# Optimization experiments

Measured on AMD Instinct MI355X. Metric: run time of the kernel, lower is better.

Reference implementation:

```python
import jax, jax.numpy as jnp
import numpy as np

B, F, L = 256, 32, 4096  # batch, num_filters, length == input_dim


def setup_inputs() -> dict:
    key = jax.random.key(0)
    k1, k2, k3 = jax.random.split(key, 3)
    x = jax.random.normal(k1, (B, L), dtype=jnp.float32)
    window_params = jax.random.normal(k2, (F, L), dtype=jnp.float32) * 0.02
    # original init: linspace(0.1, 0.5, F).unsqueeze(0); use same deterministic init
    freq_params = jnp.linspace(0.1, 0.5, F, dtype=jnp.float32)[None, :]
    return {"x": x, "window_params": window_params, "freq_params": freq_params}


def reference(x, window_params, freq_params):
    # x: [B, L]; window_params: [F, L]; freq_params: [1, F]
    length = x.shape[-1]
    windows = jax.nn.softmax(window_params, axis=-1)            # [F, L]
    freqs = jax.nn.sigmoid(freq_params)[0] * 0.5                # [F]
    n = jnp.arange(length, dtype=jnp.float32)                   # [L]
    # complex modulation atoms for ALL filters at once (single batched FFT)
    phase = -2.0 * jnp.pi * freqs[:, None] * n[None, :]         # [F, L]
    modulation = jnp.exp(1j * phase.astype(jnp.complex64))      # [F, L] complex64
    atoms = windows.astype(jnp.complex64) * modulation          # [F, L]
    Xf = jnp.fft.fft(x, axis=-1)                                # [B, L]
    Af = jnp.fft.fft(atoms, axis=-1)                            # [F, L]
    # circular correlation of x with each atom, all filters batched
    prod = Xf[:, None, :] * jnp.conj(Af)[None, :, :]            # [B, F, L]
    return jnp.real(jnp.fft.ifft(prod, axis=-1)).astype(x.dtype)  # [B, F, L]
```

## Files before the change

### kernel.cpp

```cpp
#include <hip/hip_runtime.h>
#include <math.h>

#define B 256
#define F 32
#define L 4096
#define NT 256
#define TWO_PI 6.28318530717958647692f

__device__ __forceinline__ int pidx(int i) { return i + (i >> 4); }

__device__ __forceinline__ int rev3(int i) {
    return ((i & 15) << 8) | (i & 0xF0) | (i >> 8);
}

__device__ __forceinline__ float2 cmul(float2 a, float2 b) {
    return make_float2(a.x * b.x - a.y * b.y, a.x * b.y + a.y * b.x);
}
__device__ __forceinline__ float2 cmulc(float2 a, float cr, float ci) {
    return make_float2(a.x * cr - a.y * ci, a.x * ci + a.y * cr);
}

template<int SGN>
__device__ __forceinline__ void dft4(float2& a, float2& b, float2& c, float2& d) {
    const float s = (float)SGN;
    float2 t0 = make_float2(a.x + c.x, a.y + c.y);
    float2 t1 = make_float2(a.x - c.x, a.y - c.y);
    float2 t2 = make_float2(b.x + d.x, b.y + d.y);
    float2 t3 = make_float2(b.x - d.x, b.y - d.y);
    float2 it3 = make_float2(-s * t3.y, s * t3.x);
    a = make_float2(t0.x + t2.x, t0.y + t2.y);
    c = make_float2(t0.x - t2.x, t0.y - t2.y);
    b = make_float2(t1.x + it3.x, t1.y + it3.y);
    d = make_float2(t1.x - it3.x, t1.y - it3.y);
}

template<int SGN>
__device__ __forceinline__ void dft16(float2 v[16]) {
    const float s = (float)SGN;
    const float C1 = 0.92387953251128675613f;
    const float S1 = 0.38268343236508977173f;
    const float C2 = 0.70710678118654752440f;
    #pragma unroll
    for (int c = 0; c < 4; ++c) dft4<SGN>(v[c], v[c + 4], v[c + 8], v[c + 12]);
    v[5]  = cmulc(v[5],  C1,  s * S1);
    v[6]  = cmulc(v[6],  C2,  s * C2);
    v[7]  = cmulc(v[7],  S1,  s * C1);
    v[9]  = cmulc(v[9],  C2,  s * C2);
    v[10] = make_float2(-s * v[10].y, s * v[10].x);
    v[11] = cmulc(v[11], -C2, s * C2);
    v[13] = cmulc(v[13], S1,  s * C1);
    v[14] = cmulc(v[14], -C2, s * C2);
    v[15] = cmulc(v[15], -C1, -s * S1);
    float2 o[16];
    #pragma unroll
    for (int m = 0; m < 4; ++m) {
        float2 a = v[4*m], b = v[4*m+1], c = v[4*m+2], d = v[4*m+3];
        dft4<SGN>(a, b, c, d);
        o[m] = a; o[m+4] = b; o[m+8] = c; o[m+12] = d;
    }
    #pragma unroll
    for (int i = 0; i < 16; ++i) v[i] = o[i];
}

__device__ __forceinline__ void twiddle_pow(float2 v[16], float2 w1) {
    float2 w = w1;
    #pragma unroll
    for (int q = 1; q < 16; ++q) {
        v[q] = cmul(v[q], w);
        w = cmul(w, w1);
    }
}

template<int SGN>
__device__ __forceinline__ void build_tables(float2* twp, float2* T1, int t) {
    float sv, cv;
    float a1 = (float)SGN * (TWO_PI / (float)L) * (float)t;
    sincosf(a1, &sv, &cv);
    twp[pidx(t)] = make_float2(cv, sv);
    float a2 = (float)SGN * (TWO_PI / 256.0f) * (float)((t >> 4) * (t & 15));
    sincosf(a2, &sv, &cv);
    T1[17 * (t >> 4) + (t & 15)] = make_float2(cv, sv);
}

__device__ __forceinline__ void fft_dif_fwd(float2 v[16], float2* lds,
                                            const float2* twp, const float2* T1, int t) {
    dft16<-1>(v);
    twiddle_pow(v, twp[pidx(t)]);
    #pragma unroll
    for (int p = 0; p < 16; ++p) lds[pidx(t + 256 * p)] = v[p];
    __syncthreads();
    const int base = (t >> 4) * 256 + (t & 15);
    #pragma unroll
    for (int q = 0; q < 16; ++q) v[q] = lds[pidx(base + 16 * q)];
    dft16<-1>(v);
    {
        const float2* Tr = T1 + 17 * (t & 15);
        #pragma unroll
        for (int p = 1; p < 16; ++p) v[p] = cmul(v[p], Tr[p]);
    }
    #pragma unroll
    for (int p = 0; p < 16; ++p) lds[pidx(base + 16 * p)] = v[p];
    __syncthreads();
    #pragma unroll
    for (int q = 0; q < 16; ++q) v[q] = lds[pidx(16 * t + q)];
    dft16<-1>(v);
}

__global__ void __launch_bounds__(NT) prep_kernel(const float* __restrict__ x,
                                                  const float* __restrict__ wp,
                                                  const float* __restrict__ fp,
                                                  float2* __restrict__ Xs,
                                                  float2* __restrict__ Anat) {
    __shared__ float2 lds[L + (L >> 4)];
    __shared__ float2 twp[272];
    __shared__ float2 T1[272];
    __shared__ float red[4];
    const int t = threadIdx.x;
    build_tables<-1>(twp, T1, t);
    float2 v[16];

    if (blockIdx.x < F) {
        const int f = blockIdx.x;
        const float* row = wp + (size_t)f * L;
        float rv[16];
        #pragma unroll
        for (int c = 0; c < 16; ++c) rv[c] = row[t + 256 * c];
        float m = -INFINITY;
        #pragma unroll
        for (int c = 0; c < 16; ++c) m = fmaxf(m, rv[c]);
        #pragma unroll
        for (int off = 32; off; off >>= 1) m = fmaxf(m, __shfl_down(m, off));
        if ((t & 63) == 0) red[t >> 6] = m;
        __syncthreads();
        m = fmaxf(fmaxf(red[0], red[1]), fmaxf(red[2], red[3]));
        __syncthreads();
        float s = 0.0f;
        #pragma unroll
        for (int c = 0; c < 16; ++c) { rv[c] = expf(rv[c] - m); s += rv[c]; }
        #pragma unroll
        for (int off = 32; off; off >>= 1) s += __shfl_down(s, off);
        if ((t & 63) == 0) red[t >> 6] = s;
        __syncthreads();
        s = red[0] + red[1] + red[2] + red[3];
        const float inv = 1.0f / s;
        const float fr = 0.5f / (1.0f + expf(-fp[f]));
        const float w0 = -TWO_PI * fr;
        #pragma unroll
        for (int c = 0; c < 16; ++c) {
            const int n = t + 256 * c;
            const float e = rv[c] * inv;
            float sv, cv;
            sincosf(w0 * (float)n, &sv, &cv);
            v[c] = make_float2(e * cv, e * sv);
        }
        __syncthreads();
        fft_dif_fwd(v, lds, twp, T1, t);
        float2* an = Anat + (size_t)f * L;
        #pragma unroll
        for (int r = 0; r < 16; ++r) an[rev3(16 * t + r)] = v[r];
    } else {
        const int bb = blockIdx.x - F;
        const float* row = x + (size_t)bb * L;
        #pragma unroll
        for (int q = 0; q < 16; ++q) v[q] = make_float2(row[t + 256 * q], 0.0f);
        __syncthreads();
        fft_dif_fwd(v, lds, twp, T1, t);
        float4* o4 = (float4*)(Xs + (size_t)bb * L + 16 * t);
        #pragma unroll
        for (int h = 0; h < 8; ++h)
            o4[h] = make_float4(v[2*h].x, v[2*h].y, v[2*h+1].x, v[2*h+1].y);
    }
}

__global__ void __launch_bounds__(NT) pair_kernel(const float2* __restrict__ Anat,
                                                  float2* __restrict__ Cs) {
    const int j = blockIdx.x;
    const int t = threadIdx.x;
    const float2* a0 = Anat + (size_t)(2 * j) * L;
    const float2* a1 = a0 + L;
    const float sc = 0.5f / (float)L;
    float2* co = Cs + (size_t)j * L;
    #pragma unroll
    for (int c = 0; c < 16; ++c) {
        const int i = t + 256 * c;
        const int k = rev3(i);
        const int km = (L - k) & (L - 1);
        const float2 a0k = a0[k], a0m = a0[km];
        const float2 a1k = a1[k], a1m = a1[km];
        const float g0r = a0k.x + a0m.x, g0i = a0m.y - a0k.y;
        const float g1r = a1k.x + a1m.x, g1i = a1m.y - a1k.y;
        co[i] = make_float2((g0r - g1i) * sc, (g0i + g1r) * sc);
    }
}

__global__ void __launch_bounds__(NT) corr_kernel(const float2* __restrict__ Xs,
                                                  const float2* __restrict__ Cs,
                                                  float* __restrict__ out) {
    __shared__ float2 lds[L + (L >> 4)];
    __shared__ float2 twp[272];
    __shared__ float2 T1[272];
    const int blk = blockIdx.x;
    const int b = blk >> 4;
    const int jf = blk & 15;
    const int t = threadIdx.x;
    build_tables<1>(twp, T1, t);

    const float2* xr = Xs + (size_t)b * L;
    const float2* cr = Cs + (size_t)jf * L;

    float2 v[16];
    const float4* x4 = (const float4*)(xr + 16 * t);
    const float4* c4 = (const float4*)(cr + 16 * t);
    #pragma unroll
    for (int h = 0; h < 8; ++h) {
        const float4 xa = x4[h];
        const float4 ca = c4[h];
        v[2*h]   = cmul(make_float2(xa.x, xa.y), make_float2(ca.x, ca.y));
        v[2*h+1] = cmul(make_float2(xa.z, xa.w), make_float2(ca.z, ca.w));
    }
    dft16<1>(v);
    #pragma unroll
    for (int r = 0; r < 16; ++r) lds[pidx(16 * t + r)] = v[r];
    __syncthreads();
    {
        const int base = (t >> 4) * 256 + (t & 15);
        const float2* Tr = T1 + 17 * (t & 15);
        #pragma unroll
        for (int q = 0; q < 16; ++q) v[q] = lds[pidx(base + 16 * q)];
        #pragma unroll
        for (int q = 1; q < 16; ++q) v[q] = cmul(v[q], Tr[q]);
        dft16<1>(v);
        #pragma unroll
        for (int r = 0; r < 16; ++r) lds[pidx(base + 16 * r)] = v[r];
    }
    __syncthreads();
    {
        #pragma unroll
        for (int q = 0; q < 16; ++q) v[q] = lds[pidx(t + 256 * q)];
        twiddle_pow(v, twp[pidx(t)]);
        dft16<1>(v);
        float* o0 = out + ((size_t)b * F + 2 * jf) * L;
        float* o1 = o0 + L;
        #pragma unroll
        for (int r = 0; r < 16; ++r) {
            __builtin_nontemporal_store(v[r].x, o0 + t + 256 * r);
            __builtin_nontemporal_store(v[r].y, o1 + t + 256 * r);
        }
    }
}

extern "C" void kernel_launch(void* const* d_in, const int* in_sizes, int n_in,
                              void* d_out, int out_size, void* d_ws, size_t ws_size,
                              hipStream_t stream) {
    (void)in_sizes; (void)n_in; (void)out_size; (void)ws_size;
    const float* x  = (const float*)d_in[0];
    const float* wp = (const float*)d_in[1];
    const float* fp = (const float*)d_in[2];
    float* out = (float*)d_out;

    float2* Xs   = (float2*)d_ws;
    float2* Cs   = Xs + (size_t)B * L;
    float2* Anat = Cs + (size_t)(F / 2) * L;

    prep_kernel<<<dim3(F + B), dim3(NT), 0, stream>>>(x, wp, fp, Xs, Anat);
    pair_kernel<<<dim3(F / 2), dim3(NT), 0, stream>>>(Anat, Cs);
    corr_kernel<<<dim3(B * F / 2), dim3(NT), 0, stream>>>(Xs, Cs, out);
}
```

Before: 186.3 us.

## Fuse atom pairing into prep kernel and process two filter pairs per corr block

```diff
diff --git a/kernel.cpp b/kernel.cpp
--- a/kernel.cpp
+++ b/kernel.cpp
@@ -110,56 +110,75 @@
                                                   const float* __restrict__ wp,
                                                   const float* __restrict__ fp,
                                                   float2* __restrict__ Xs,
-                                                  float2* __restrict__ Anat) {
+                                                  float2* __restrict__ Cs) {
     __shared__ float2 lds[L + (L >> 4)];
     __shared__ float2 twp[272];
     __shared__ float2 T1[272];
+    __shared__ float2 bufa[L];
+    __shared__ float2 bufb[L];
     __shared__ float red[4];
     const int t = threadIdx.x;
     build_tables<-1>(twp, T1, t);
     float2 v[16];
 
-    if (blockIdx.x < F) {
-        const int f = blockIdx.x;
-        const float* row = wp + (size_t)f * L;
-        float rv[16];
-        #pragma unroll
-        for (int c = 0; c < 16; ++c) rv[c] = row[t + 256 * c];
-        float m = -INFINITY;
-        #pragma unroll
-        for (int c = 0; c < 16; ++c) m = fmaxf(m, rv[c]);
-        #pragma unroll
-        for (int off = 32; off; off >>= 1) m = fmaxf(m, __shfl_down(m, off));
-        if ((t & 63) == 0) red[t >> 6] = m;
-        __syncthreads();
-        m = fmaxf(fmaxf(red[0], red[1]), fmaxf(red[2], red[3]));
-        __syncthreads();
-        float s = 0.0f;
-        #pragma unroll
-        for (int c = 0; c < 16; ++c) { rv[c] = expf(rv[c] - m); s += rv[c]; }
-        #pragma unroll
-        for (int off = 32; off; off >>= 1) s += __shfl_down(s, off);
-        if ((t & 63) == 0) red[t >> 6] = s;
-        __syncthreads();
-        s = red[0] + red[1] + red[2] + red[3];
-        const float inv = 1.0f / s;
-        const float fr = 0.5f / (1.0f + expf(-fp[f]));
-        const float w0 = -TWO_PI * fr;
+    if (blockIdx.x < F / 2) {
+        const int j = blockIdx.x;
+        for (int half = 0; half < 2; ++half) {
+            const int f = 2 * j + half;
+            const float* row = wp + (size_t)f * L;
+            float rv[16];
+            #pragma unroll
+            for (int c = 0; c < 16; ++c) rv[c] = row[t + 256 * c];
+            float m = -INFINITY;
+            #pragma unroll
+            for (int c = 0; c < 16; ++c) m = fmaxf(m, rv[c]);
+            #pragma unroll
+            for (int off = 32; off; off >>= 1) m = fmaxf(m, __shfl_down(m, off));
+            if ((t & 63) == 0) red[t >> 6] = m;
+            __syncthreads();
+            m = fmaxf(fmaxf(red[0], red[1]), fmaxf(red[2], red[3]));
+            __syncthreads();
+            float s = 0.0f;
+            #pragma unroll
+            for (int c = 0; c < 16; ++c) { rv[c] = expf(rv[c] - m); s += rv[c]; }
+            #pragma unroll
+            for (int off = 32; off; off >>= 1) s += __shfl_down(s, off);
+            if ((t & 63) == 0) red[t >> 6] = s;
+            __syncthreads();
+            s = red[0] + red[1] + red[2] + red[3];
+            const float inv = 1.0f / s;
+            const float fr = 0.5f / (1.0f + expf(-fp[f]));
+            const float w0 = -TWO_PI * fr;
+            #pragma unroll
+            for (int c = 0; c < 16; ++c) {
+                const int n = t + 256 * c;
+                const float e = rv[c] * inv;
+                float sv, cv;
+                sincosf(w0 * (float)n, &sv, &cv);
+                v[c] = make_float2(e * cv, e * sv);
+            }
+            __syncthreads();
+            fft_dif_fwd(v, lds, twp, T1, t);
+            float2* buf = half ? bufb : bufa;
+            #pragma unroll
+            for (int r = 0; r < 16; ++r) buf[rev3(16 * t + r)] = v[r];
+            __syncthreads();
+        }
+        const float sc = 0.5f / (float)L;
+        float2* co = Cs + (size_t)j * L;
         #pragma unroll
         for (int c = 0; c < 16; ++c) {
-            const int n = t + 256 * c;
-            const float e = rv[c] * inv;
-            float sv, cv;
-            sincosf(w0 * (float)n, &sv, &cv);
-            v[c] = make_float2(e * cv, e * sv);
-        }
-        __syncthreads();
-        fft_dif_fwd(v, lds, twp, T1, t);
-        float2* an = Anat + (size_t)f * L;
-        #pragma unroll
-        for (int r = 0; r < 16; ++r) an[rev3(16 * t + r)] = v[r];
+            const int i = t + 256 * c;
+            const int k = rev3(i);
+            const int km = (L - k) & (L - 1);
+            const float2 a0k = bufa[k], a0m = bufa[km];
+            const float2 a1k = bufb[k], a1m = bufb[km];
+            const float g0r = a0k.x + a0m.x, g0i = a0m.y - a0k.y;
+            const float g1r = a1k.x + a1m.x, g1i = a1m.y - a1k.y;
+            co[i] = make_float2((g0r - g1i) * sc, (g0i + g1r) * sc);
+        }
     } else {
-        const int bb = blockIdx.x - F;
+        const int bb = blockIdx.x - F / 2;
         const float* row = x + (size_t)bb * L;
         #pragma unroll
         for (int q = 0; q < 16; ++q) v[q] = make_float2(row[t + 256 * q], 0.0f);
@@ -169,27 +188,6 @@
         #pragma unroll
         for (int h = 0; h < 8; ++h)
             o4[h] = make_float4(v[2*h].x, v[2*h].y, v[2*h+1].x, v[2*h+1].y);
-    }
-}
-
-__global__ void __launch_bounds__(NT) pair_kernel(const float2* __restrict__ Anat,
-                                                  float2* __restrict__ Cs) {
-    const int j = blockIdx.x;
-    const int t = threadIdx.x;
-    const float2* a0 = Anat + (size_t)(2 * j) * L;
-    const float2* a1 = a0 + L;
-    const float sc = 0.5f / (float)L;
-    float2* co = Cs + (size_t)j * L;
-    #pragma unroll
-    for (int c = 0; c < 16; ++c) {
-        const int i = t + 256 * c;
-        const int k = rev3(i);
-        const int km = (L - k) & (L - 1);
-        const float2 a0k = a0[k], a0m = a0[km];
-        const float2 a1k = a1[k], a1m = a1[km];
-        const float g0r = a0k.x + a0m.x, g0i = a0m.y - a0k.y;
-        const float g1r = a1k.x + a1m.x, g1i = a1m.y - a1k.y;
-        co[i] = make_float2((g0r - g1i) * sc, (g0i + g1r) * sc);
     }
 }
 
@@ -200,43 +198,55 @@
     __shared__ float2 twp[272];
     __shared__ float2 T1[272];
     const int blk = blockIdx.x;
-    const int b = blk >> 4;
-    const int jf = blk & 15;
+    const int rest = blk >> 3;
+    const int jf8 = rest & 7;
+    const int b = ((rest >> 3) << 3) | (blk & 7);
     const int t = threadIdx.x;
     build_tables<1>(twp, T1, t);
 
-    const float2* xr = Xs + (size_t)b * L;
-    const float2* cr = Cs + (size_t)jf * L;
-
-    float2 v[16];
-    const float4* x4 = (const float4*)(xr + 16 * t);
-    const float4* c4 = (const float4*)(cr + 16 * t);
-    #pragma unroll
-    for (int h = 0; h < 8; ++h) {
-        const float4 xa = x4[h];
-        const float4 ca = c4[h];
-        v[2*h]   = cmul(make_float2(xa.x, xa.y), make_float2(ca.x, ca.y));
-        v[2*h+1] = cmul(make_float2(xa.z, xa.w), make_float2(ca.z, ca.w));
-    }
-    dft16<1>(v);
-    #pragma unroll
-    for (int r = 0; r < 16; ++r) lds[pidx(16 * t + r)] = v[r];
-    __syncthreads();
+    float2 xv[16];
     {
-        const int base = (t >> 4) * 256 + (t & 15);
-        const float2* Tr = T1 + 17 * (t & 15);
-        #pragma unroll
-        for (int q = 0; q < 16; ++q) v[q] = lds[pidx(base + 16 * q)];
-        #pragma unroll
-        for (int q = 1; q < 16; ++q) v[q] = cmul(v[q], Tr[q]);
+        const float4* x4 = (const float4*)(Xs + (size_t)b * L + 16 * t);
+        #pragma unroll
+        for (int h = 0; h < 8; ++h) {
+            const float4 xa = x4[h];
+            xv[2*h]   = make_float2(xa.x, xa.y);
+            xv[2*h+1] = make_float2(xa.z, xa.w);
+        }
+    }
+
+    #pragma unroll
+    for (int ff = 0; ff < 2; ++ff) {
+        const int jf = jf8 + 8 * ff;
+        float2 v[16];
+        {
+            const float4* c4 = (const float4*)(Cs + (size_t)jf * L + 16 * t);
+            #pragma unroll
+            for (int h = 0; h < 8; ++h) {
+                const float4 ca = c4[h];
+                v[2*h]   = cmul(xv[2*h],   make_float2(ca.x, ca.y));
+                v[2*h+1] = cmul(xv[2*h+1], make_float2(ca.z, ca.w));
+            }
+        }
         dft16<1>(v);
         #pragma unroll
-        for (int r = 0; r < 16; ++r) lds[pidx(base + 16 * r)] = v[r];
-    }
-    __syncthreads();
-    {
+        for (int r = 0; r < 16; ++r) lds[pidx(16 * t + r)] = v[r];
+        __syncthreads();
+        {
+            const int base = (t >> 4) * 256 + (t & 15);
+            const float2* Tr = T1 + 17 * (t & 15);
+            #pragma unroll
+            for (int q = 0; q < 16; ++q) v[q] = lds[pidx(base + 16 * q)];
+            #pragma unroll
+            for (int q = 1; q < 16; ++q) v[q] = cmul(v[q], Tr[q]);
+            dft16<1>(v);
+            #pragma unroll
+            for (int r = 0; r < 16; ++r) lds[pidx(base + 16 * r)] = v[r];
+        }
+        __syncthreads();
         #pragma unroll
         for (int q = 0; q < 16; ++q) v[q] = lds[pidx(t + 256 * q)];
+        if (ff == 0) __syncthreads();
         twiddle_pow(v, twp[pidx(t)]);
         dft16<1>(v);
         float* o0 = out + ((size_t)b * F + 2 * jf) * L;
@@ -258,11 +268,9 @@
     const float* fp = (const float*)d_in[2];
     float* out = (float*)d_out;
 
-    float2* Xs   = (float2*)d_ws;
-    float2* Cs   = Xs + (size_t)B * L;
-    float2* Anat = Cs + (size_t)(F / 2) * L;
-
-    prep_kernel<<<dim3(F + B), dim3(NT), 0, stream>>>(x, wp, fp, Xs, Anat);
-    pair_kernel<<<dim3(F / 2), dim3(NT), 0, stream>>>(Anat, Cs);
-    corr_kernel<<<dim3(B * F / 2), dim3(NT), 0, stream>>>(Xs, Cs, out);
-}
+    float2* Xs = (float2*)d_ws;
+    float2* Cs = Xs + (size_t)B * L;
+
+    prep_kernel<<<dim3(F / 2 + B), dim3(NT), 0, stream>>>(x, wp, fp, Xs, Cs);
+    corr_kernel<<<dim3(B * F / 4), dim3(NT), 0, stream>>>(Xs, Cs, out);
+}
```

Result: no change. 185.6 us (-0.4%).
